# Kernel tuning notes

Measured on AMD Instinct MI355X. Metric: run time of the kernel, lower is better.

The kernel has to match this reference:

```python
import jax, jax.numpy as jnp
import numpy as np

B, C, H, W = 2, 256, 192, 192
STRIDE = 8


def conv2d(x, w, b, pad_h, pad_w):
    y = jax.lax.conv_general_dilated(
        x, w, window_strides=(1, 1),
        padding=[(pad_h, pad_h), (pad_w, pad_w)],
        dimension_numbers=('NCHW', 'OIHW', 'NCHW'))
    return y + b[None, :, None, None]


def rotated_feature_align(feat, boxes, spatial_scale):
    # feat: [B,C,Hf,Wf]; boxes: [B,Hf*Wf,5] per-pixel rboxes in image coords.
    # points=1: bilinearly sample feat at each pixel's box center and add to feat,
    # matching mmcv's rotated_feature_align forward kernel (incl. its (y,x) read order
    # and ROI-Align-style border handling).
    Bf, Cf, Hf, Wf = feat.shape
    y = boxes[..., 0].reshape(Bf, Hf, Wf) * spatial_scale
    x = boxes[..., 1].reshape(Bf, Hf, Wf) * spatial_scale
    valid = (y >= -1.0) & (y <= Hf) & (x >= -1.0) & (x <= Wf)
    y = jnp.maximum(y, 0.0)
    x = jnp.maximum(x, 0.0)
    yl0 = jnp.floor(y).astype(jnp.int32)
    xl0 = jnp.floor(x).astype(jnp.int32)
    ey = yl0 >= Hf - 1
    ex = xl0 >= Wf - 1
    yl = jnp.where(ey, Hf - 1, yl0)
    yh = jnp.where(ey, Hf - 1, jnp.minimum(yl0 + 1, Hf - 1))
    xl = jnp.where(ex, Wf - 1, xl0)
    xh = jnp.where(ex, Wf - 1, jnp.minimum(xl0 + 1, Wf - 1))
    y = jnp.where(ey, jnp.asarray(Hf - 1, feat.dtype), y)
    x = jnp.where(ex, jnp.asarray(Wf - 1, feat.dtype), x)
    ly = y - yl.astype(feat.dtype)
    lx = x - xl.astype(feat.dtype)
    hy = 1.0 - ly
    hx = 1.0 - lx
    ft = jnp.transpose(feat, (0, 2, 3, 1))  # [B,Hf,Wf,C]
    bi = jnp.arange(Bf)[:, None, None]
    v = ((hy * hx)[..., None] * ft[bi, yl, xl]
         + (hy * lx)[..., None] * ft[bi, yl, xh]
         + (ly * hx)[..., None] * ft[bi, yh, xl]
         + (ly * lx)[..., None] * ft[bi, yh, xh])
    v = jnp.where(valid[..., None], v, 0.0)
    return feat + jnp.transpose(v, (0, 3, 1, 2))


def setup_inputs() -> dict:
    key = jax.random.key(0)
    ks = jax.random.split(key, 9)
    x = jax.random.normal(ks[0], (B, C, H, W), dtype=jnp.float32)
    img = float(H * STRIDE)
    cy = jax.random.uniform(ks[1], (B, H * W), minval=0.0, maxval=img)
    cx = jax.random.uniform(ks[2], (B, H * W), minval=0.0, maxval=img)
    bw = jax.random.uniform(ks[3], (B, H * W), minval=8.0, maxval=64.0)
    bh = jax.random.uniform(ks[4], (B, H * W), minval=8.0, maxval=64.0)
    ba = jax.random.uniform(ks[5], (B, H * W), minval=-np.pi / 2, maxval=np.pi / 2)
    best_rbboxes = jnp.stack([cy, cx, bw, bh, ba], axis=-1)  # [B, H*W, 5]
    std = 0.01  # normal_init(std=0.01)
    w51 = jax.random.normal(ks[6], (C, C, 5, 1), dtype=jnp.float32) * std
    w15 = jax.random.normal(ks[7], (C, C, 1, 5), dtype=jnp.float32) * std
    w11 = jax.random.normal(ks[8], (C, C, 1, 1), dtype=jnp.float32) * std
    b51 = jnp.zeros((C,), jnp.float32)
    b15 = jnp.zeros((C,), jnp.float32)
    b11 = jnp.zeros((C,), jnp.float32)
    return {"x": x, "best_rbboxes": best_rbboxes, "w51": w51, "b51": b51,
            "w15": w15, "b15": b15, "w11": w11, "b11": b11}


def reference(x, best_rbboxes, w51, b51, w15, b15, w11, b11):
    # conv_5_1(conv_1_5(x)) + conv_1_1(x), then rotated feature alignment, then residual.
    feat = conv2d(conv2d(x, w15, b15, 0, 2), w51, b51, 2, 0) + conv2d(x, w11, b11, 0, 0)
    refined = rotated_feature_align(feat, best_rbboxes, 1.0 / STRIDE)
    return x + refined
```

## Files before the change

kernel.cpp:

```cpp
#include <hip/hip_runtime.h>
#include <hip/hip_bf16.h>
#include <stdint.h>

#define B_ 2
#define C_ 256
#define H_ 192
#define W_ 192
#define HW_ (H_*W_)
#define CHW_ (C_*HW_)
#define P_ (B_*HW_)
#define SCALE 0.125f

typedef __attribute__((ext_vector_type(8))) short bf16x8;
typedef __attribute__((ext_vector_type(4))) float f32x4;

__device__ __forceinline__ void gload_lds16(const void* g, void* l) {
  __builtin_amdgcn_global_load_lds(
      (const __attribute__((address_space(1))) uint32_t*)g,
      (__attribute__((address_space(3))) uint32_t*)l, 16, 0, 0);
}

__global__ __launch_bounds__(256) void wtrans_kernel(
    const float* __restrict__ w15, const float* __restrict__ w51,
    const float* __restrict__ w11,
    __hip_bfloat16* __restrict__ w1t, __hip_bfloat16* __restrict__ w2t,
    __hip_bfloat16* __restrict__ zbuf) {
  int i = blockIdx.x * 256 + threadIdx.x;
  if (i < C_ * C_ * 5) {
    int co = i / (C_ * 5);
    int r  = i - co * (C_ * 5);
    int ci = r / 5;
    int k  = r - ci * 5;
    w1t[(size_t)co * 1280 + k * 256 + ci] = __float2bfloat16(w15[i]);
    w2t[(size_t)co * 1536 + k * 256 + ci] = __float2bfloat16(w51[i]);
  }
  if (i < C_ * C_) {
    int co = i >> 8, ci = i & 255;
    w2t[(size_t)co * 1536 + 1280 + ci] = __float2bfloat16(w11[i]);
  }
  if (i < 1024) zbuf[i] = __float2bfloat16(0.f);
}

__global__ __launch_bounds__(256) void nchw2nhwc_kernel(
    const float* __restrict__ x, __hip_bfloat16* __restrict__ xT) {
  __shared__ float tile[32][33];
  int p0 = blockIdx.x * 32, c0 = blockIdx.y * 32, b = blockIdx.z;
  int tx = threadIdx.x, ty = threadIdx.y;
  const float* xb = x + (size_t)b * CHW_;
#pragma unroll
  for (int j = 0; j < 4; ++j)
    tile[ty + j * 8][tx] = xb[(size_t)(c0 + ty + j * 8) * HW_ + p0 + tx];
  __syncthreads();
  __hip_bfloat16* xo = xT + (size_t)b * HW_ * C_;
#pragma unroll
  for (int j = 0; j < 4; ++j)
    xo[(size_t)(p0 + ty + j * 8) * C_ + c0 + tx] = __float2bfloat16(tile[tx][ty + j * 8]);
}

#define AB1 25600
__global__ __launch_bounds__(256, 3) void gemm1_kernel(
    const __hip_bfloat16* __restrict__ xT, const __hip_bfloat16* __restrict__ w1t,
    const float* __restrict__ b15, __hip_bfloat16* __restrict__ t1,
    const __hip_bfloat16* __restrict__ zbuf) {
  __shared__ __align__(16) char lds[AB1 + 16384];
  int bid = blockIdx.x;
  bid = (bid & 7) * 96 + (bid >> 3);
  const int nb = bid & 1, bh = bid >> 1;
  const int p0 = bh * 192;
  const int tid = threadIdx.x, l = tid & 63, wid = tid >> 6;
  const int wrow = (wid >> 1) * 96, wcol = (wid & 1) * 64;
  const int sboff = (((l & 7) ^ (l >> 3)) << 4);
  const int lrow = l >> 3;
  const int corow0 = nb * 128;

  int b_ad[4][2];
#pragma unroll
  for (int n = 0; n < 4; ++n)
#pragma unroll
    for (int kk = 0; kk < 2; ++kk)
      b_ad[n][kk] = AB1 + (wcol + n * 16 + (l & 15)) * 128 +
                    (((kk * 4 + (l >> 4)) ^ ((l & 15) & 7)) << 4);

  f32x4 acc[6][4] = {};
  const char* xTb = (const char*)xT;
  const char* wB  = (const char*)w1t;
  const char* zb  = (const char*)zbuf;

  for (int cib = 0; cib < 4; ++cib) {
    for (int is = wid; is < 25; is += 4) {
      int row = is * 8 + lrow;
      const char* src = ((unsigned)(row - 4) < 192u)
          ? xTb + (size_t)(p0 + row - 4) * 512 + cib * 128 + sboff
          : zb + sboff;
      gload_lds16(src, lds + is * 1024);
    }
    for (int k = 0; k < 5; ++k) {
      int boff = k * 512 + cib * 128;
#pragma unroll
      for (int ii = 0; ii < 4; ++ii) {
        int is = wid * 4 + ii;
        const char* bs = wB + (size_t)(corow0 + is * 8 + lrow) * 2560 + boff + sboff;
        gload_lds16(bs, lds + AB1 + is * 1024);
      }
      __syncthreads();
      int x8 = ((l & 15) + k + 2) & 7;
      int arow0 = wrow + (l & 15) + k + 2;
#pragma unroll
      for (int kk = 0; kk < 2; ++kk) {
        int ablk = ((kk * 4 + (l >> 4)) ^ x8) << 4;
        bf16x8 bfr[4];
#pragma unroll
        for (int n = 0; n < 4; ++n) bfr[n] = *(const bf16x8*)(lds + b_ad[n][kk]);
#pragma unroll
        for (int m = 0; m < 6; ++m) {
          bf16x8 af = *(const bf16x8*)(lds + (arow0 + m * 16) * 128 + ablk);
#pragma unroll
          for (int n = 0; n < 4; ++n)
            acc[m][n] = __builtin_amdgcn_mfma_f32_16x16x32_bf16(af, bfr[n], acc[m][n], 0, 0, 0);
        }
      }
      __syncthreads();
    }
  }
#pragma unroll
  for (int n = 0; n < 4; ++n) {
    int co = corow0 + wcol + n * 16 + (l & 15);
    float bias = b15[co];
#pragma unroll
    for (int m = 0; m < 6; ++m) {
      int prow = p0 + wrow + m * 16 + (l >> 4) * 4;
#pragma unroll
      for (int r = 0; r < 4; ++r)
        t1[(size_t)(prow + r) * 256 + co] = __float2bfloat16(acc[m][n][r] + bias);
    }
  }
}

#define AB2 24576
__global__ __launch_bounds__(256, 3) void gemm2_kernel(
    const __hip_bfloat16* __restrict__ t1, const __hip_bfloat16* __restrict__ xT,
    const __hip_bfloat16* __restrict__ w2t,
    const float* __restrict__ b51, const float* __restrict__ b11,
    __hip_bfloat16* __restrict__ featT, const __hip_bfloat16* __restrict__ zbuf) {
  __shared__ __align__(16) char lds[AB2 + 16384];
  int bid = blockIdx.x;
  bid = (bid & 7) * 96 + (bid >> 3);
  const int nb = bid & 1, bh = bid >> 1;
  const int p0 = bh * 192;
  const int h = bh % 192;
  const int tid = threadIdx.x, l = tid & 63, wid = tid >> 6;
  const int wrow = (wid >> 1) * 96, wcol = (wid & 1) * 64;
  const int sboff = (((l & 7) ^ (l >> 3)) << 4);
  const int lrow = l >> 3;
  const int corow0 = nb * 128;

  int a_ad[6][2], b_ad[4][2];
#pragma unroll
  for (int m = 0; m < 6; ++m)
#pragma unroll
    for (int kk = 0; kk < 2; ++kk)
      a_ad[m][kk] = (wrow + m * 16 + (l & 15)) * 128 +
                    (((kk * 4 + (l >> 4)) ^ ((l & 15) & 7)) << 4);
#pragma unroll
  for (int n = 0; n < 4; ++n)
#pragma unroll
    for (int kk = 0; kk < 2; ++kk)
      b_ad[n][kk] = AB2 + (wcol + n * 16 + (l & 15)) * 128 +
                    (((kk * 4 + (l >> 4)) ^ ((l & 15) & 7)) << 4);

  f32x4 acc[6][4] = {};
  const char* t1b = (const char*)t1;
  const char* xTb = (const char*)xT;
  const char* wB  = (const char*)w2t;
  const char* zb  = (const char*)zbuf;

  for (int s = 0; s < 24; ++s) {
    const char* abase;
    int boff;
    if (s < 20) {
      int k = s >> 2, cib = s & 3, dl = k - 2;
      abase = ((unsigned)(h + dl) < 192u)
          ? t1b + (size_t)(p0 + dl * 192) * 512 + cib * 128
          : (const char*)0;
      boff = k * 512 + cib * 128;
    } else {
      abase = xTb + (size_t)p0 * 512 + (s - 20) * 128;
      boff = 2560 + (s - 20) * 128;
    }
    for (int is = wid; is < 24; is += 4) {
      int row = is * 8 + lrow;
      const char* src = abase ? abase + (size_t)row * 512 + sboff : zb + sboff;
      gload_lds16(src, lds + is * 1024);
    }
#pragma unroll
    for (int ii = 0; ii < 4; ++ii) {
      int is = wid * 4 + ii;
      const char* bs = wB + (size_t)(corow0 + is * 8 + lrow) * 3072 + boff + sboff;
      gload_lds16(bs, lds + AB2 + is * 1024);
    }
    __syncthreads();
#pragma unroll
    for (int kk = 0; kk < 2; ++kk) {
      bf16x8 bfr[4];
#pragma unroll
      for (int n = 0; n < 4; ++n) bfr[n] = *(const bf16x8*)(lds + b_ad[n][kk]);
#pragma unroll
      for (int m = 0; m < 6; ++m) {
        bf16x8 af = *(const bf16x8*)(lds + a_ad[m][kk]);
#pragma unroll
        for (int n = 0; n < 4; ++n)
          acc[m][n] = __builtin_amdgcn_mfma_f32_16x16x32_bf16(af, bfr[n], acc[m][n], 0, 0, 0);
      }
    }
    __syncthreads();
  }
#pragma unroll
  for (int n = 0; n < 4; ++n) {
    int co = corow0 + wcol + n * 16 + (l & 15);
    float bias = b51[co] + b11[co];
#pragma unroll
    for (int m = 0; m < 6; ++m) {
      int prow = p0 + wrow + m * 16 + (l >> 4) * 4;
#pragma unroll
      for (int r = 0; r < 4; ++r)
        featT[(size_t)(prow + r) * 256 + co] = __float2bfloat16(acc[m][n][r] + bias);
    }
  }
}

__global__ __launch_bounds__(256) void align_kernel(
    const __hip_bfloat16* __restrict__ xT, const __hip_bfloat16* __restrict__ featT,
    const float* __restrict__ boxes, float* __restrict__ out) {
  __shared__ float vs[32][258];
  const int tid = threadIdx.x, l = tid & 63, wv = tid >> 6;
  const int p0 = blockIdx.x * 32;

#pragma unroll 4
  for (int i = 0; i < 8; ++i) {
    int pl = wv * 8 + i;
    int p = p0 + pl;
    int b = p / HW_;
    int p2 = p - b * HW_;
    float yy = boxes[(size_t)p * 5 + 0] * SCALE;
    float xx = boxes[(size_t)p * 5 + 1] * SCALE;
    bool valid = (yy >= -1.0f) && (yy <= (float)H_) && (xx >= -1.0f) && (xx <= (float)W_);
    yy = fmaxf(yy, 0.f);
    xx = fmaxf(xx, 0.f);
    int yl = (int)floorf(yy), xl = (int)floorf(xx);
    int yh, xh;
    if (yl >= H_ - 1) { yl = H_ - 1; yh = H_ - 1; yy = (float)(H_ - 1); } else { yh = yl + 1; }
    if (xl >= W_ - 1) { xl = W_ - 1; xh = W_ - 1; xx = (float)(W_ - 1); } else { xh = xl + 1; }
    float ly = yy - (float)yl, lx = xx - (float)xl;
    float hy = 1.f - ly, hx = 1.f - lx;
    float q00 = hy * hx, q01 = hy * lx, q10 = ly * hx, q11 = ly * lx;
    if (!valid) { q00 = 0.f; q01 = 0.f; q10 = 0.f; q11 = 0.f; }
    const unsigned short* fT = (const unsigned short*)featT + (size_t)b * HW_ * C_;
    const unsigned short* xb = (const unsigned short*)xT + (size_t)b * HW_ * C_;
    int co = l * 4;
    uint2 A  = *(const uint2*)(fT + ((size_t)yl * W_ + xl) * C_ + co);
    uint2 Bv = *(const uint2*)(fT + ((size_t)yl * W_ + xh) * C_ + co);
    uint2 Cv = *(const uint2*)(fT + ((size_t)yh * W_ + xl) * C_ + co);
    uint2 D  = *(const uint2*)(fT + ((size_t)yh * W_ + xh) * C_ + co);
    uint2 E  = *(const uint2*)(fT + (size_t)p2 * C_ + co);
    uint2 X  = *(const uint2*)(xb + (size_t)p2 * C_ + co);
    float o[4];
#pragma unroll
    for (int w = 0; w < 2; ++w) {
      unsigned int aw = (&A.x)[w], bw = (&Bv.x)[w], cw = (&Cv.x)[w],
                   dw = (&D.x)[w], ew = (&E.x)[w], xw = (&X.x)[w];
      float a0 = __uint_as_float(aw << 16), a1 = __uint_as_float(aw & 0xffff0000u);
      float b0 = __uint_as_float(bw << 16), b1 = __uint_as_float(bw & 0xffff0000u);
      float c0 = __uint_as_float(cw << 16), c1 = __uint_as_float(cw & 0xffff0000u);
      float d0 = __uint_as_float(dw << 16), d1 = __uint_as_float(dw & 0xffff0000u);
      float e0 = __uint_as_float(ew << 16), e1 = __uint_as_float(ew & 0xffff0000u);
      float x0 = __uint_as_float(xw << 16), x1 = __uint_as_float(xw & 0xffff0000u);
      o[w * 2 + 0] = x0 + e0 + q00 * a0 + q01 * b0 + q10 * c0 + q11 * d0;
      o[w * 2 + 1] = x1 + e1 + q00 * a1 + q01 * b1 + q10 * c1 + q11 * d1;
    }
    *(float2*)&vs[pl][co]     = make_float2(o[0], o[1]);
    *(float2*)&vs[pl][co + 2] = make_float2(o[2], o[3]);
  }
  __syncthreads();

  const int pl = tid & 31, cg = tid >> 5;
  const int p = p0 + pl;
  const int b = p / HW_;
  const int p2 = p - b * HW_;
  float* oc = out + (size_t)b * CHW_ + p2;
#pragma unroll
  for (int j = 0; j < 32; ++j) {
    int ch = cg * 32 + j;
    __builtin_nontemporal_store(vs[pl][ch], &oc[(size_t)ch * HW_]);
  }
}

extern "C" void kernel_launch(void* const* d_in, const int* in_sizes, int n_in,
                              void* d_out, int out_size, void* d_ws, size_t ws_size,
                              hipStream_t stream) {
  const float* x     = (const float*)d_in[0];
  const float* boxes = (const float*)d_in[1];
  const float* w51   = (const float*)d_in[2];
  const float* b51   = (const float*)d_in[3];
  const float* w15   = (const float*)d_in[4];
  const float* b15   = (const float*)d_in[5];
  const float* w11   = (const float*)d_in[6];
  const float* b11   = (const float*)d_in[7];
  float* out = (float*)d_out;

  __hip_bfloat16* featT = (__hip_bfloat16*)d_ws;
  __hip_bfloat16* xT   = featT + (size_t)P_ * C_;
  __hip_bfloat16* w1t  = xT + (size_t)P_ * C_;
  __hip_bfloat16* w2t  = w1t + (size_t)C_ * 1280;
  __hip_bfloat16* zbuf = w2t + (size_t)C_ * 1536;
  __hip_bfloat16* t1 = (__hip_bfloat16*)d_out;

  wtrans_kernel<<<dim3((C_ * C_ * 5 + 255) / 256), 256, 0, stream>>>(
      w15, w51, w11, w1t, w2t, zbuf);
  nchw2nhwc_kernel<<<dim3(HW_ / 32, C_ / 32, B_), dim3(32, 8), 0, stream>>>(x, xT);
  gemm1_kernel<<<dim3(768), 256, 0, stream>>>(xT, w1t, b15, t1, zbuf);
  gemm2_kernel<<<dim3(768), 256, 0, stream>>>(t1, xT, w2t, b51, b11, featT, zbuf);
  align_kernel<<<dim3(P_ / 32), 256, 0, stream>>>(xT, featT, boxes, out);
}
```

Measured before the change: 173.2 us.

## Double-buffer gemm2 LDS stages and split tile across eight waves

gemm2 now runs with 512 threads (8 waves), each wave covering 48 rows instead of 96, so per-wave accumulators shrink. LDS is double-buffered: the next A stage is issued before the current compute and the next B stage between the two k-halves, with manual vmcnt waits and raw barriers replacing the two __syncthreads per step. MFMA bursts are wrapped in setprio. The goal is to overlap global-to-LDS loads with MFMA work and hide latency better. The cost is 80KB of LDS per block, which may limit occupancy, and fragile hand-written waitcnt ordering.

```diff
diff --git a/kernel.cpp b/kernel.cpp
--- a/kernel.cpp
+++ b/kernel.cpp
@@ -136,90 +136,120 @@
   }
 }
 
-#define AB2 24576
-__global__ __launch_bounds__(256, 3) void gemm2_kernel(
+#define A2SZ 24576
+#define B2OFF 49152
+__global__ __launch_bounds__(512, 4) void gemm2_kernel(
     const __hip_bfloat16* __restrict__ t1, const __hip_bfloat16* __restrict__ xT,
     const __hip_bfloat16* __restrict__ w2t,
     const float* __restrict__ b51, const float* __restrict__ b11,
     __hip_bfloat16* __restrict__ featT, const __hip_bfloat16* __restrict__ zbuf) {
-  __shared__ __align__(16) char lds[AB2 + 16384];
+  __shared__ __align__(16) char lds[81920];
   int bid = blockIdx.x;
   bid = (bid & 7) * 96 + (bid >> 3);
   const int nb = bid & 1, bh = bid >> 1;
   const int p0 = bh * 192;
   const int h = bh % 192;
   const int tid = threadIdx.x, l = tid & 63, wid = tid >> 6;
-  const int wrow = (wid >> 1) * 96, wcol = (wid & 1) * 64;
+  const int wrow = (wid >> 1) * 48, wcol = (wid & 1) * 64;
   const int sboff = (((l & 7) ^ (l >> 3)) << 4);
   const int lrow = l >> 3;
   const int corow0 = nb * 128;
 
-  int a_ad[6][2], b_ad[4][2];
-#pragma unroll
-  for (int m = 0; m < 6; ++m)
-#pragma unroll
-    for (int kk = 0; kk < 2; ++kk)
-      a_ad[m][kk] = (wrow + m * 16 + (l & 15)) * 128 +
-                    (((kk * 4 + (l >> 4)) ^ ((l & 15) & 7)) << 4);
-#pragma unroll
-  for (int n = 0; n < 4; ++n)
-#pragma unroll
-    for (int kk = 0; kk < 2; ++kk)
-      b_ad[n][kk] = AB2 + (wcol + n * 16 + (l & 15)) * 128 +
-                    (((kk * 4 + (l >> 4)) ^ ((l & 15) & 7)) << 4);
-
-  f32x4 acc[6][4] = {};
   const char* t1b = (const char*)t1;
   const char* xTb = (const char*)xT;
   const char* wB  = (const char*)w2t;
   const char* zb  = (const char*)zbuf;
 
-  for (int s = 0; s < 24; ++s) {
+  auto stageA = [&](int s, int buf) {
     const char* abase;
-    int boff;
     if (s < 20) {
       int k = s >> 2, cib = s & 3, dl = k - 2;
       abase = ((unsigned)(h + dl) < 192u)
           ? t1b + (size_t)(p0 + dl * 192) * 512 + cib * 128
           : (const char*)0;
-      boff = k * 512 + cib * 128;
     } else {
       abase = xTb + (size_t)p0 * 512 + (s - 20) * 128;
-      boff = 2560 + (s - 20) * 128;
-    }
-    for (int is = wid; is < 24; is += 4) {
-      int row = is * 8 + lrow;
+    }
+#pragma unroll
+    for (int i = 0; i < 3; ++i) {
+      int slot = i * 8 + wid;
+      int row = slot * 8 + lrow;
       const char* src = abase ? abase + (size_t)row * 512 + sboff : zb + sboff;
-      gload_lds16(src, lds + is * 1024);
-    }
-#pragma unroll
-    for (int ii = 0; ii < 4; ++ii) {
-      int is = wid * 4 + ii;
-      const char* bs = wB + (size_t)(corow0 + is * 8 + lrow) * 3072 + boff + sboff;
-      gload_lds16(bs, lds + AB2 + is * 1024);
-    }
-    __syncthreads();
-#pragma unroll
-    for (int kk = 0; kk < 2; ++kk) {
-      bf16x8 bfr[4];
-#pragma unroll
-      for (int n = 0; n < 4; ++n) bfr[n] = *(const bf16x8*)(lds + b_ad[n][kk]);
-#pragma unroll
-      for (int m = 0; m < 6; ++m) {
-        bf16x8 af = *(const bf16x8*)(lds + a_ad[m][kk]);
+      gload_lds16(src, lds + buf * A2SZ + slot * 1024);
+    }
+  };
+  auto stageB = [&](int s, int buf) {
+    int boff = (s < 20) ? (s >> 2) * 512 + (s & 3) * 128 : 2560 + (s - 20) * 128;
+#pragma unroll
+    for (int i = 0; i < 2; ++i) {
+      int slot = i * 8 + wid;
+      const char* bs = wB + (size_t)(corow0 + slot * 8 + lrow) * 3072 + boff + sboff;
+      gload_lds16(bs, lds + B2OFF + buf * 16384 + slot * 1024);
+    }
+  };
+
+  f32x4 acc[3][4] = {};
+  stageA(0, 0);
+  stageB(0, 0);
+  for (int t = 0; t < 24; ++t) {
+    const int cur = t & 1, nxt = cur ^ 1;
+    if (t < 23) {
+      stageA(t + 1, nxt);
+      asm volatile("s_waitcnt vmcnt(3)" ::: "memory");
+    } else {
+      asm volatile("s_waitcnt vmcnt(0)" ::: "memory");
+    }
+    __builtin_amdgcn_s_barrier();
+    __builtin_amdgcn_sched_barrier(0);
+    const char* la = lds + cur * A2SZ;
+    const char* lb = lds + B2OFF + cur * 16384;
+    {
+      bf16x8 af[3], bfr[4];
+#pragma unroll
+      for (int m = 0; m < 3; ++m)
+        af[m] = *(const bf16x8*)(la + (wrow + m * 16 + (l & 15)) * 128 +
+                 (((l >> 4) ^ ((l & 15) & 7)) << 4));
+#pragma unroll
+      for (int n = 0; n < 4; ++n)
+        bfr[n] = *(const bf16x8*)(lb + (wcol + n * 16 + (l & 15)) * 128 +
+                 (((l >> 4) ^ ((l & 15) & 7)) << 4));
+      __builtin_amdgcn_s_setprio(1);
+#pragma unroll
+      for (int m = 0; m < 3; ++m)
 #pragma unroll
         for (int n = 0; n < 4; ++n)
-          acc[m][n] = __builtin_amdgcn_mfma_f32_16x16x32_bf16(af, bfr[n], acc[m][n], 0, 0, 0);
-      }
-    }
-    __syncthreads();
+          acc[m][n] = __builtin_amdgcn_mfma_f32_16x16x32_bf16(af[m], bfr[n], acc[m][n], 0, 0, 0);
+      __builtin_amdgcn_s_setprio(0);
+    }
+    if (t < 23) stageB(t + 1, nxt);
+    {
+      bf16x8 af[3], bfr[4];
+#pragma unroll
+      for (int m = 0; m < 3; ++m)
+        af[m] = *(const bf16x8*)(la + (wrow + m * 16 + (l & 15)) * 128 +
+                 (((4 + (l >> 4)) ^ ((l & 15) & 7)) << 4));
+#pragma unroll
+      for (int n = 0; n < 4; ++n)
+        bfr[n] = *(const bf16x8*)(lb + (wcol + n * 16 + (l & 15)) * 128 +
+                 (((4 + (l >> 4)) ^ ((l & 15) & 7)) << 4));
+      __builtin_amdgcn_s_setprio(1);
+#pragma unroll
+      for (int m = 0; m < 3; ++m)
+#pragma unroll
+        for (int n = 0; n < 4; ++n)
+          acc[m][n] = __builtin_amdgcn_mfma_f32_16x16x32_bf16(af[m], bfr[n], acc[m][n], 0, 0, 0);
+      __builtin_amdgcn_s_setprio(0);
+    }
+    __builtin_amdgcn_sched_barrier(0);
+    __builtin_amdgcn_s_barrier();
+    __builtin_amdgcn_sched_barrier(0);
   }
 #pragma unroll
   for (int n = 0; n < 4; ++n) {
     int co = corow0 + wcol + n * 16 + (l & 15);
     float bias = b51[co] + b11[co];
 #pragma unroll
-    for (int m = 0; m < 6; ++m) {
+    for (int m = 0; m < 3; ++m) {
       int prow = p0 + wrow + m * 16 + (l >> 4) * 4;
 #pragma unroll
       for (int r = 0; r < 4; ++r)
@@ -318,6 +348,6 @@
       w15, w51, w11, w1t, w2t, zbuf);
   nchw2nhwc_kernel<<<dim3(HW_ / 32, C_ / 32, B_), dim3(32, 8), 0, stream>>>(x, xT);
   gemm1_kernel<<<dim3(768), 256, 0, stream>>>(xT, w1t, b15, t1, zbuf);
-  gemm2_kernel<<<dim3(768), 256, 0, stream>>>(t1, xT, w2t, b51, b11, featT, zbuf);
+  gemm2_kernel<<<dim3(768), 512, 0, stream>>>(t1, xT, w2t, b51, b11, featT, zbuf);
   align_kernel<<<dim3(P_ / 32), 256, 0, stream>>>(xT, featT, boxes, out);
 }
```

Result: no change. 172.6 us (-0.3%).
